# Kernel tuning notes

Hardware: AMD Instinct MI355X
Metric: run time of the kernel (lower is better)

The kernel has to match this reference:

```python
import jax, jax.numpy as jnp
import numpy as np

N_NODES = 10000
LN_EPS = 1e-5


def _gcn(x, W, b, src, dst):
    # GraphConvolution: linear transform then sum-aggregate messages over edges.
    sup = x @ W                               # [B, N, H]
    msg = sup[:, src, :]                      # [B, E, H] gather from source nodes
    agg = jax.vmap(lambda m: jax.ops.segment_sum(m, dst, num_segments=N_NODES))(msg)
    return agg + b


def _layernorm(x, g, b):
    mu = jnp.mean(x, axis=-1, keepdims=True)
    var = jnp.var(x, axis=-1, keepdims=True)
    return (x - mu) * jax.lax.rsqrt(var + LN_EPS) * g + b


def _attention_pool(x, W, u, num_iterations=3):
    # x: [B, N, d] -> r: [B, 1, d]
    a = jnp.tanh(x @ W) @ u                   # [B, N]
    alpha = jax.nn.softmax(a, axis=1)
    r = jnp.einsum('bn,bnd->bd', alpha, x)
    for _ in range(num_iterations):
        beta = jax.nn.softmax(jnp.einsum('bnd,bd->bn', x, r), axis=1)
        r = jnp.einsum('bn,bnd->bd', beta, x)
    return r[:, None, :]


def _forward(x, src, dst, W_conv0, b_conv0, W_convs, b_convs,
             mW1, mb1, mW2, mb2, mW3, mb3,
             ln1_g, ln1_b, ln2_g, ln2_b, attnW, attnu, fW1, fb1, fW2, fb2,
             fcW, fcb):
    gelu = lambda t: jax.nn.gelu(t, approximate=False)
    # stacked GCN layers (first layer distinct input dim)
    x = gelu(_gcn(x, W_conv0, b_conv0, src, dst))
    for i in range(W_convs.shape[0]):
        x = gelu(_gcn(x, W_convs[i], b_convs[i], src, dst))
    # dropout is identity in eval mode
    # MLP head
    x = jax.nn.relu(x @ mW1 + mb1)
    x = jax.nn.relu(x @ mW2 + mb2)
    x = x @ mW3 + mb3
    # Encoder: 2 layers of (attention-pool residual + LN + FFN residual + LN)
    for i in range(2):
        x = x + _attention_pool(x, attnW[i], attnu[i])   # broadcast [B,1,d]
        x = _layernorm(x, ln1_g[i], ln1_b[i])
        h = jax.nn.relu(x @ fW1[i] + fb1[i]) @ fW2[i] + fb2[i]
        x = _layernorm(x + h, ln2_g[i], ln2_b[i])
    x = x @ fcW + fcb                          # [B, N, out]
    return x.mean(axis=1)                      # [B, out]


def setup_inputs() -> dict:
    key = jax.random.key(0)
    ks = jax.random.split(key, 32)
    B, N, E = 4, N_NODES, 160000
    F_in, H, D, A, OUT = 128, 256, 256, 8, 10
    s = lambda k, *shape: jax.random.normal(k, shape, jnp.float32) * 0.05
    return {
        'x': jax.random.normal(ks[0], (B, N, F_in), jnp.float32),
        'src': jax.random.randint(ks[1], (E,), 0, N, jnp.int32),
        'dst': jax.random.randint(ks[2], (E,), 0, N, jnp.int32),
        'W_conv0': s(ks[3], F_in, H), 'b_conv0': s(ks[4], H),
        'W_convs': s(ks[5], 3, H, H), 'b_convs': s(ks[6], 3, H),
        'mW1': s(ks[7], H, H // 2), 'mb1': s(ks[8], H // 2),
        'mW2': s(ks[9], H // 2, H // 4), 'mb2': s(ks[10], H // 4),
        'mW3': s(ks[11], H // 4, D), 'mb3': s(ks[12], D),
        'ln1_g': jnp.ones((2, D), jnp.float32), 'ln1_b': jnp.zeros((2, D), jnp.float32),
        'ln2_g': jnp.ones((2, D), jnp.float32), 'ln2_b': jnp.zeros((2, D), jnp.float32),
        'attnW': s(ks[13], 2, D, A), 'attnu': s(ks[14], 2, A),
        'fW1': s(ks[15], 2, D, H), 'fb1': s(ks[16], 2, H),
        'fW2': s(ks[17], 2, H, D), 'fb2': s(ks[18], 2, D),
        'fcW': s(ks[19], D, OUT), 'fcb': s(ks[20], OUT),
    }


def reference(x, src, dst, W_conv0, b_conv0, W_convs, b_convs,
              mW1, mb1, mW2, mb2, mW3, mb3,
              ln1_g, ln1_b, ln2_g, ln2_b, attnW, attnu, fW1, fb1, fW2, fb2,
              fcW, fcb):
    return _forward(x, src, dst, W_conv0, b_conv0, W_convs, b_convs,
                    mW1, mb1, mW2, mb2, mW3, mb3,
                    ln1_g, ln1_b, ln2_g, ln2_b, attnW, attnu, fW1, fb1, fW2, fb2,
                    fcW, fcb)
```

## Files before the change

### kernel.cpp

```cpp
#include <hip/hip_runtime.h>
#include <math.h>

#define NN 10000
#define NB 4
#define NE 160000
#define DM 256
#define MR (NB * NN)
#define LN_EPS 1e-5f
#define WCHUNK 100
#define NCH (NN / WCHUNK)

typedef __attribute__((ext_vector_type(8))) short short8;
typedef __attribute__((ext_vector_type(8))) unsigned short us8;
typedef __attribute__((ext_vector_type(4))) float floatx4;


__device__ inline float bf2f(unsigned short u) {
    unsigned int x = ((unsigned int)u) << 16;
    float f;
    __builtin_memcpy(&f, &x, 4);
    return f;
}

__device__ inline unsigned short f2bf(float f) {
    unsigned int x;
    __builtin_memcpy(&x, &f, 4);
    unsigned int r = x + 0x7FFFu + ((x >> 16) & 1u);
    return (unsigned short)(r >> 16);
}

__device__ inline float gelu_exact(float x) {
    return 0.5f * x * (1.0f + erff(x * 0.70710678118654752f));
}

__device__ inline float waveAllReduce(float v) {
#pragma unroll
    for (int off = 32; off > 0; off >>= 1) v += __shfl_xor(v, off, 64);
    return v;
}

__device__ inline void gld16(const unsigned short* g, unsigned short* l) {
    __builtin_amdgcn_global_load_lds((const __attribute__((address_space(1))) void*)g,
                                     (__attribute__((address_space(3))) void*)l, 16, 0, 0);
}


__global__ void zero_f32_kernel(float* p, int n) {
    int i = blockIdx.x * 256 + threadIdx.x;
    if (i < n) p[i] = 0.0f;
}

__global__ void zero_i32_kernel(int* p, int n) {
    int i = blockIdx.x * 256 + threadIdx.x;
    if (i < n) p[i] = 0;
}

__global__ void cvt_bf16_kernel(const float* __restrict__ in, unsigned short* __restrict__ out, int n) {
    int i = blockIdx.x * 256 + threadIdx.x;
    if (i < n) out[i] = f2bf(in[i]);
}

struct TD { const float* src; unsigned short* dst; int K; int N; };
struct TDs { TD d[11]; };

__global__ void transpose_all_kernel(TDs tds) {
    TD t = tds.d[blockIdx.y];
    int idx = blockIdx.x * 256 + threadIdx.x;
    int total = t.K * t.N;
    if (idx < total) {
        int n = idx / t.K;
        int k = idx - n * t.K;
        t.dst[idx] = f2bf(t.src[(size_t)k * t.N + n]);
    }
}


__global__ void hist_kernel(const int* __restrict__ dst, int* __restrict__ counts, int e) {
    int i = blockIdx.x * 256 + threadIdx.x;
    if (i < e) atomicAdd(&counts[dst[i]], 1);
}

__global__ __launch_bounds__(256) void scan_kernel(const int* __restrict__ counts,
                                                   int* __restrict__ row_ptr,
                                                   int* __restrict__ fill_pos, int n) {
    __shared__ int sums[256];
    int tid = threadIdx.x;
    int chunk = (n + 255) / 256;
    int s0 = tid * chunk;
    int s1 = min(n, s0 + chunk);
    int local = 0;
    for (int i = s0; i < s1; i++) local += counts[i];
    sums[tid] = local;
    __syncthreads();
    for (int off = 1; off < 256; off <<= 1) {
        int v = (tid >= off) ? sums[tid - off] : 0;
        __syncthreads();
        sums[tid] += v;
        __syncthreads();
    }
    int base = (tid == 0) ? 0 : sums[tid - 1];
    for (int i = s0; i < s1; i++) {
        row_ptr[i] = base;
        fill_pos[i] = base;
        base += counts[i];
    }
    if (tid == 255) row_ptr[n] = sums[255];
}

__global__ void fill_kernel(const int* __restrict__ src, const int* __restrict__ dst,
                            int* __restrict__ fill_pos, int* __restrict__ csr_src, int e) {
    int i = blockIdx.x * 256 + threadIdx.x;
    if (i < e) {
        int p = atomicAdd(&fill_pos[dst[i]], 1);
        csr_src[p] = src[i];
    }
}


template <int BN, int CM>
__global__ __launch_bounds__(256) void mfma_gemm_kernel(
    const unsigned short* __restrict__ A, const unsigned short* __restrict__ Bt,
    const float* __restrict__ bias, void* __restrict__ Cp, int K, int N, int act) {
    constexpr int NBF = BN / 32;
    __shared__ unsigned short AsL[4 * 64 * 8];
    __shared__ unsigned short BsL[(BN / 16) * 64 * 8];

    const int tid = threadIdx.x;
    const int w = tid >> 6, l = tid & 63;
    const int wm = w >> 1, wn = w & 1;
    const int bm0 = blockIdx.y * 64;
    const int bn0 = blockIdx.x * BN;
    const int lm = l & 15, lq = l >> 4;

    floatx4 acc[2][NBF];
#pragma unroll
    for (int mi = 0; mi < 2; mi++)
#pragma unroll
        for (int ni = 0; ni < NBF; ni++) acc[mi][ni] = (floatx4){0.f, 0.f, 0.f, 0.f};

    const int s_ll = tid & 63;
    const int a_row = bm0 + (tid >> 6) * 16 + (s_ll & 15);
    const int s_kc = (s_ll >> 4) * 8;

    for (int k0 = 0; k0 < K; k0 += 32) {
        gld16(&A[(size_t)a_row * K + k0 + s_kc], &AsL[tid * 8]);
#pragma unroll
        for (int cc = 0; cc < BN / 64; cc++) {
            int c = tid + cc * 256;
            int rown = bn0 + (c >> 6) * 16 + (c & 15);
            int kc = k0 + ((c & 63) >> 4) * 8;
            gld16(&Bt[(size_t)rown * K + kc], &BsL[c * 8]);
        }
        __syncthreads();
        short8 af[2], bfv[NBF];
#pragma unroll
        for (int mi = 0; mi < 2; mi++) af[mi] = *(short8*)&AsL[((wm * 2 + mi) * 64 + l) * 8];
#pragma unroll
        for (int ni = 0; ni < NBF; ni++) bfv[ni] = *(short8*)&BsL[((wn * NBF + ni) * 64 + l) * 8];
#pragma unroll
        for (int mi = 0; mi < 2; mi++)
#pragma unroll
            for (int ni = 0; ni < NBF; ni++)
                acc[mi][ni] = __builtin_amdgcn_mfma_f32_16x16x32_bf16(af[mi], bfv[ni], acc[mi][ni], 0, 0, 0);
        __syncthreads();
    }

#pragma unroll
    for (int ni = 0; ni < NBF; ni++) {
        int col = bn0 + (wn * NBF + ni) * 16 + lm;
        float bv = bias ? bias[col] : 0.0f;
#pragma unroll
        for (int mi = 0; mi < 2; mi++) {
            int row0 = bm0 + (wm * 2 + mi) * 16 + lq * 4;
#pragma unroll
            for (int r = 0; r < 4; r++) {
                int row = row0 + r;
                float v = acc[mi][ni][r] + bv;
                if (act) v = fmaxf(v, 0.0f);
                if (CM == 0) {
                    ((float*)Cp)[(size_t)row * N + col] = v;
                } else if (CM == 1) {
                    ((unsigned short*)Cp)[(size_t)row * N + col] = f2bf(v);
                } else {
                    int bb = row / NN;
                    int nn = row - bb * NN;
                    ((unsigned short*)Cp)[(size_t)nn * (NB * DM) + bb * DM + col] = f2bf(v);
                }
            }
        }
    }
}


__global__ __launch_bounds__(256) void agg_kernel(const unsigned short* __restrict__ sup,
                                                  const int* __restrict__ row_ptr,
                                                  const int* __restrict__ csr_src,
                                                  const float* __restrict__ bias,
                                                  unsigned short* __restrict__ out) {
    int half = threadIdx.x >> 7;
    int n = blockIdx.x * 2 + half;
    int t = threadIdx.x & 127;
    int s = row_ptr[n], e = row_ptr[n + 1];
    float acc[8] = {0.f, 0.f, 0.f, 0.f, 0.f, 0.f, 0.f, 0.f};
    int j = s;
    for (; j + 4 <= e; j += 4) {
        int s0 = csr_src[j], s1 = csr_src[j + 1], s2 = csr_src[j + 2], s3 = csr_src[j + 3];
        us8 v0 = *(const us8*)&sup[(size_t)s0 * (NB * DM) + t * 8];
        us8 v1 = *(const us8*)&sup[(size_t)s1 * (NB * DM) + t * 8];
        us8 v2 = *(const us8*)&sup[(size_t)s2 * (NB * DM) + t * 8];
        us8 v3 = *(const us8*)&sup[(size_t)s3 * (NB * DM) + t * 8];
#pragma unroll
        for (int k = 0; k < 8; k++)
            acc[k] += (bf2f(v0[k]) + bf2f(v1[k])) + (bf2f(v2[k]) + bf2f(v3[k]));
    }
    for (; j < e; j++) {
        us8 v = *(const us8*)&sup[(size_t)csr_src[j] * (NB * DM) + t * 8];
#pragma unroll
        for (int k = 0; k < 8; k++) acc[k] += bf2f(v[k]);
    }
    int b = t >> 5, d0 = (t & 31) * 8;
    us8 o;
#pragma unroll
    for (int k = 0; k < 8; k++) o[k] = f2bf(gelu_exact(acc[k] + bias[d0 + k]));
    *(us8*)&out[((size_t)b * NN + n) * DM + d0] = o;
}


__global__ __launch_bounds__(256) void attn_score_kernel(const unsigned short* __restrict__ x16,
                                                         const float* __restrict__ W,
                                                         const float* __restrict__ u,
                                                         float* __restrict__ s) {
    int l = threadIdx.x & 63, w = threadIdx.x >> 6;
    int idx = blockIdx.x * 4 + w;
    ushort4 xb = *(const ushort4*)&x16[(size_t)idx * DM + l * 4];
    float xs[4] = {bf2f(xb.x), bf2f(xb.y), bf2f(xb.z), bf2f(xb.w)};
    const float4* Wv = (const float4*)W;
    int d0 = l * 4;
    float t[8] = {0, 0, 0, 0, 0, 0, 0, 0};
#pragma unroll
    for (int dd = 0; dd < 4; dd++) {
        float4 w0 = Wv[(d0 + dd) * 2 + 0];
        float4 w1 = Wv[(d0 + dd) * 2 + 1];
        t[0] += xs[dd] * w0.x; t[1] += xs[dd] * w0.y; t[2] += xs[dd] * w0.z; t[3] += xs[dd] * w0.w;
        t[4] += xs[dd] * w1.x; t[5] += xs[dd] * w1.y; t[6] += xs[dd] * w1.z; t[7] += xs[dd] * w1.w;
    }
#pragma unroll
    for (int j = 0; j < 8; j++) t[j] = waveAllReduce(t[j]);
    if (l == 0) {
        float acc = 0.0f;
#pragma unroll
        for (int j = 0; j < 8; j++) acc += tanhf(t[j]) * u[j];
        s[idx] = acc;
    }
}

__global__ __launch_bounds__(256) void dot_kernel(const unsigned short* __restrict__ x16,
                                                  const float* __restrict__ r,
                                                  float* __restrict__ s) {
    int l = threadIdx.x & 63, w = threadIdx.x >> 6;
    int idx = blockIdx.x * 4 + w;
    int b = idx / NN;
    ushort4 xb = *(const ushort4*)&x16[(size_t)idx * DM + l * 4];
    float4 rv = *(const float4*)&r[b * DM + l * 4];
    float acc = bf2f(xb.x) * rv.x + bf2f(xb.y) * rv.y + bf2f(xb.z) * rv.z + bf2f(xb.w) * rv.w;
    acc = waveAllReduce(acc);
    if (l == 0) s[idx] = acc;
}

__global__ __launch_bounds__(256) void attn_pool_kernel(const unsigned short* __restrict__ x16,
                                                        const float* __restrict__ sarr,
                                                        float* __restrict__ pm,
                                                        float* __restrict__ pl,
                                                        float* __restrict__ pv) {
    int c = blockIdx.x, b = blockIdx.y;
    int tid = threadIdx.x, w = tid >> 6, l = tid & 63;
    int n0 = c * WCHUNK;
    float m = -INFINITY, L = 0.0f;
    float v0 = 0.f, v1 = 0.f, v2 = 0.f, v3 = 0.f;
    for (int n = n0 + w; n < n0 + WCHUNK; n += 4) {
        float s = sarr[b * NN + n];
        ushort4 xb = *(const ushort4*)&x16[((size_t)b * NN + n) * DM + l * 4];
        float x0 = bf2f(xb.x), x1 = bf2f(xb.y), x2 = bf2f(xb.z), x3 = bf2f(xb.w);
        if (s > m) {
            float sc = __expf(m - s);
            L *= sc; v0 *= sc; v1 *= sc; v2 *= sc; v3 *= sc;
            m = s;
        }
        float wgt = __expf(s - m);
        L += wgt;
        v0 += wgt * x0; v1 += wgt * x1; v2 += wgt * x2; v3 += wgt * x3;
    }
    __shared__ float sm[4], sl[4];
    __shared__ float sv[4][DM];
    if (l == 0) { sm[w] = m; sl[w] = L; }
    float4 vv = {v0, v1, v2, v3};
    *(float4*)&sv[w][l * 4] = vv;
    __syncthreads();
    int d = tid;
    float M = fmaxf(fmaxf(sm[0], sm[1]), fmaxf(sm[2], sm[3]));
    float e0 = __expf(sm[0] - M), e1 = __expf(sm[1] - M);
    float e2 = __expf(sm[2] - M), e3 = __expf(sm[3] - M);
    float Lt = e0 * sl[0] + e1 * sl[1] + e2 * sl[2] + e3 * sl[3];
    float vd = e0 * sv[0][d] + e1 * sv[1][d] + e2 * sv[2][d] + e3 * sv[3][d];
    pv[((size_t)b * NCH + c) * DM + d] = vd;
    if (d == 0) {
        pm[b * NCH + c] = M;
        pl[b * NCH + c] = Lt;
    }
}

__global__ __launch_bounds__(256) void attn_combine_kernel(const float* __restrict__ pm,
                                                           const float* __restrict__ pl,
                                                           const float* __restrict__ pv,
                                                           float* __restrict__ r) {
    int b = blockIdx.x, tid = threadIdx.x;
    __shared__ float red[256];
    __shared__ float se[NCH];
    float mv = (tid < NCH) ? pm[b * NCH + tid] : -INFINITY;
    red[tid] = mv;
    __syncthreads();
    for (int off = 128; off > 0; off >>= 1) {
        if (tid < off) red[tid] = fmaxf(red[tid], red[tid + off]);
        __syncthreads();
    }
    float M = red[0];
    __syncthreads();
    float e = (tid < NCH) ? __expf(mv - M) : 0.0f;
    if (tid < NCH) se[tid] = e;
    red[tid] = (tid < NCH) ? e * pl[b * NCH + tid] : 0.0f;
    __syncthreads();
    for (int off = 128; off > 0; off >>= 1) {
        if (tid < off) red[tid] += red[tid + off];
        __syncthreads();
    }
    float L = red[0];
    __syncthreads();
    float acc = 0.0f;
    for (int c = 0; c < NCH; c++) acc += se[c] * pv[((size_t)b * NCH + c) * DM + tid];
    r[b * DM + tid] = acc / L;
}


__global__ __launch_bounds__(256) void ln_bcast_kernel(const unsigned short* __restrict__ x16,
                                                       const float* __restrict__ r,
                                                       const float* __restrict__ g,
                                                       const float* __restrict__ bt,
                                                       unsigned short* __restrict__ out16) {
    int l = threadIdx.x & 63, w = threadIdx.x >> 6;
    int row = blockIdx.x * 4 + w;
    int b = row / NN;
    ushort4 xb = *(const ushort4*)&x16[(size_t)row * DM + l * 4];
    float4 rv = *(const float4*)(r + (size_t)b * DM + l * 4);
    float4 y;
    y.x = bf2f(xb.x) + rv.x; y.y = bf2f(xb.y) + rv.y;
    y.z = bf2f(xb.z) + rv.z; y.w = bf2f(xb.w) + rv.w;
    float s = y.x + y.y + y.z + y.w;
    float sq = y.x * y.x + y.y * y.y + y.z * y.z + y.w * y.w;
    s = waveAllReduce(s);
    sq = waveAllReduce(sq);
    float mean = s * (1.0f / 256.0f);
    float var = sq * (1.0f / 256.0f) - mean * mean;
    float rstd = rsqrtf(var + LN_EPS);
    float4 gv = *(const float4*)(g + l * 4);
    float4 bv = *(const float4*)(bt + l * 4);
    ushort4 o;
    o.x = f2bf((y.x - mean) * rstd * gv.x + bv.x);
    o.y = f2bf((y.y - mean) * rstd * gv.y + bv.y);
    o.z = f2bf((y.z - mean) * rstd * gv.z + bv.z);
    o.w = f2bf((y.w - mean) * rstd * gv.w + bv.w);
    *(ushort4*)&out16[(size_t)row * DM + l * 4] = o;
}

__global__ __launch_bounds__(256) void ln_elem_kernel(const unsigned short* __restrict__ x16,
                                                      const float* __restrict__ h,
                                                      const float* __restrict__ g,
                                                      const float* __restrict__ bt,
                                                      unsigned short* __restrict__ out16) {
    int l = threadIdx.x & 63, w = threadIdx.x >> 6;
    int row = blockIdx.x * 4 + w;
    ushort4 xb = *(const ushort4*)&x16[(size_t)row * DM + l * 4];
    float4 hv = *(const float4*)(h + (size_t)row * DM + l * 4);
    float4 y;
    y.x = bf2f(xb.x) + hv.x; y.y = bf2f(xb.y) + hv.y;
    y.z = bf2f(xb.z) + hv.z; y.w = bf2f(xb.w) + hv.w;
    float s = y.x + y.y + y.z + y.w;
    float sq = y.x * y.x + y.y * y.y + y.z * y.z + y.w * y.w;
    s = waveAllReduce(s);
    sq = waveAllReduce(sq);
    float mean = s * (1.0f / 256.0f);
    float var = sq * (1.0f / 256.0f) - mean * mean;
    float rstd = rsqrtf(var + LN_EPS);
    float4 gv = *(const float4*)(g + l * 4);
    float4 bv = *(const float4*)(bt + l * 4);
    ushort4 o;
    o.x = f2bf((y.x - mean) * rstd * gv.x + bv.x);
    o.y = f2bf((y.y - mean) * rstd * gv.y + bv.y);
    o.z = f2bf((y.z - mean) * rstd * gv.z + bv.z);
    o.w = f2bf((y.w - mean) * rstd * gv.w + bv.w);
    *(ushort4*)&out16[(size_t)row * DM + l * 4] = o;
}


__global__ __launch_bounds__(256) void colsum_kernel(const unsigned short* __restrict__ x16,
                                                     float* __restrict__ cs) {
    int b = blockIdx.y, c = blockIdx.x, d = threadIdx.x;
    int n0 = c * WCHUNK, n1 = n0 + WCHUNK;
    float acc = 0.0f;
    for (int n = n0; n < n1; n++) acc += bf2f(x16[((size_t)b * NN + n) * DM + d]);
    atomicAdd(&cs[b * DM + d], acc);
}

__global__ __launch_bounds__(64) void final_kernel(const float* __restrict__ cs,
                                                   const float* __restrict__ fcW,
                                                   const float* __restrict__ fcb,
                                                   float* __restrict__ out) {
    int b = blockIdx.x;
    int o = threadIdx.x;
    if (o < 10) {
        float acc = 0.0f;
        for (int d = 0; d < DM; d++) acc += cs[b * DM + d] * fcW[d * 10 + o];
        out[b * 10 + o] = acc * (1.0f / NN) + fcb[o];
    }
}


extern "C" void kernel_launch(void* const* d_in, const int* in_sizes, int n_in,
                              void* d_out, int out_size, void* d_ws, size_t ws_size,
                              hipStream_t stream) {
    const float* x_in    = (const float*)d_in[0];
    const int*   src     = (const int*)d_in[1];
    const int*   dst     = (const int*)d_in[2];
    const float* W_conv0 = (const float*)d_in[3];
    const float* b_conv0 = (const float*)d_in[4];
    const float* W_convs = (const float*)d_in[5];
    const float* b_convs = (const float*)d_in[6];
    const float* mW1 = (const float*)d_in[7];
    const float* mb1 = (const float*)d_in[8];
    const float* mW2 = (const float*)d_in[9];
    const float* mb2 = (const float*)d_in[10];
    const float* mW3 = (const float*)d_in[11];
    const float* mb3 = (const float*)d_in[12];
    const float* ln1_g = (const float*)d_in[13];
    const float* ln1_b = (const float*)d_in[14];
    const float* ln2_g = (const float*)d_in[15];
    const float* ln2_b = (const float*)d_in[16];
    const float* attnW = (const float*)d_in[17];
    const float* attnu = (const float*)d_in[18];
    const float* fW1 = (const float*)d_in[19];
    const float* fb1 = (const float*)d_in[20];
    const float* fW2 = (const float*)d_in[21];
    const float* fb2 = (const float*)d_in[22];
    const float* fcW = (const float*)d_in[23];
    const float* fcb = (const float*)d_in[24];
    float* out = (float*)d_out;

    char* p = (char*)d_ws;
    auto alloc = [&](size_t bytes) { char* q = p; p += (bytes + 255) & ~(size_t)255; return q; };
    float* A = (float*)alloc((size_t)MR * DM * 4);
    unsigned short* sup16 = (unsigned short*)alloc((size_t)MR * DM * 2);
    unsigned short* act16 = (unsigned short*)alloc((size_t)MR * DM * 2);
    unsigned short* b16   = (unsigned short*)alloc((size_t)MR * DM * 2);
    unsigned short* t1    = (unsigned short*)alloc((size_t)MR * 128 * 2);
    unsigned short* t2    = (unsigned short*)alloc((size_t)MR * 64 * 2);
    unsigned short* wt    = (unsigned short*)alloc((size_t)548864 * 2);
    float* a_score = (float*)alloc((size_t)MR * 4);
    float* rbuf = (float*)alloc(NB * DM * 4);
    float* pm0  = (float*)alloc(NB * NCH * 4);
    float* pl0  = (float*)alloc(NB * NCH * 4);
    float* pv0  = (float*)alloc((size_t)NB * NCH * DM * 4);
    float* colsum = (float*)alloc(NB * DM * 4);
    int* counts   = (int*)alloc(NN * 4);
    int* row_ptr  = (int*)alloc((NN + 1) * 4);
    int* fill_pos = (int*)alloc(NN * 4);
    int* csr_src  = (int*)alloc(NE * 4);

    unsigned short* Wt_conv0 = wt;
    unsigned short* Wt_convs = Wt_conv0 + 32768;
    unsigned short* mW1t = Wt_convs + 196608;
    unsigned short* mW2t = mW1t + 32768;
    unsigned short* mW3t = mW2t + 8192;
    unsigned short* fW1t = mW3t + 16384;
    unsigned short* fW2t = fW1t + 131072;

    const dim3 blk(256);

    zero_i32_kernel<<<(NN + 255) / 256, blk, 0, stream>>>(counts, NN);
    hist_kernel<<<(NE + 255) / 256, blk, 0, stream>>>(dst, counts, NE);
    scan_kernel<<<1, blk, 0, stream>>>(counts, row_ptr, fill_pos, NN);
    fill_kernel<<<(NE + 255) / 256, blk, 0, stream>>>(src, dst, fill_pos, csr_src, NE);

    TDs tds;
    tds.d[0]  = {W_conv0, Wt_conv0, 128, 256};
    tds.d[1]  = {W_convs + 0 * 65536, Wt_convs + 0 * 65536, 256, 256};
    tds.d[2]  = {W_convs + 1 * 65536, Wt_convs + 1 * 65536, 256, 256};
    tds.d[3]  = {W_convs + 2 * 65536, Wt_convs + 2 * 65536, 256, 256};
    tds.d[4]  = {mW1, mW1t, 256, 128};
    tds.d[5]  = {mW2, mW2t, 128, 64};
    tds.d[6]  = {mW3, mW3t, 64, 256};
    tds.d[7]  = {fW1 + 0 * 65536, fW1t + 0 * 65536, 256, 256};
    tds.d[8]  = {fW1 + 1 * 65536, fW1t + 1 * 65536, 256, 256};
    tds.d[9]  = {fW2 + 0 * 65536, fW2t + 0 * 65536, 256, 256};
    tds.d[10] = {fW2 + 1 * 65536, fW2t + 1 * 65536, 256, 256};
    transpose_all_kernel<<<dim3(256, 11), blk, 0, stream>>>(tds);

    cvt_bf16_kernel<<<(MR * 128 + 255) / 256, blk, 0, stream>>>(x_in, t1, MR * 128);

    mfma_gemm_kernel<128, 2><<<dim3(2, MR / 64), blk, 0, stream>>>(t1, Wt_conv0, nullptr, sup16, 128, 256, 0);
    agg_kernel<<<NN / 2, blk, 0, stream>>>(sup16, row_ptr, csr_src, b_conv0, act16);
    for (int i = 0; i < 3; i++) {
        mfma_gemm_kernel<128, 2><<<dim3(2, MR / 64), blk, 0, stream>>>(act16, Wt_convs + (size_t)i * 65536, nullptr, sup16, 256, 256, 0);
        agg_kernel<<<NN / 2, blk, 0, stream>>>(sup16, row_ptr, csr_src, b_convs + (size_t)i * 256, act16);
    }

    mfma_gemm_kernel<128, 1><<<dim3(1, MR / 64), blk, 0, stream>>>(act16, mW1t, mb1, t1, 256, 128, 1);
    mfma_gemm_kernel<64, 1><<<dim3(1, MR / 64), blk, 0, stream>>>(t1, mW2t, mb2, t2, 128, 64, 1);
    mfma_gemm_kernel<128, 1><<<dim3(2, MR / 64), blk, 0, stream>>>(t2, mW3t, mb3, act16, 64, 256, 0);

    const dim3 poolGrid(NCH, NB);
    for (int i = 0; i < 2; i++) {
        const float* Wp = attnW + (size_t)i * DM * 8;
        const float* up = attnu + (size_t)i * 8;
        attn_score_kernel<<<MR / 4, blk, 0, stream>>>(act16, Wp, up, a_score);
        attn_pool_kernel<<<poolGrid, blk, 0, stream>>>(act16, a_score, pm0, pl0, pv0);
        attn_combine_kernel<<<NB, blk, 0, stream>>>(pm0, pl0, pv0, rbuf);
        for (int it = 0; it < 3; it++) {
            dot_kernel<<<MR / 4, blk, 0, stream>>>(act16, rbuf, a_score);
            attn_pool_kernel<<<poolGrid, blk, 0, stream>>>(act16, a_score, pm0, pl0, pv0);
            attn_combine_kernel<<<NB, blk, 0, stream>>>(pm0, pl0, pv0, rbuf);
        }
        ln_bcast_kernel<<<MR / 4, blk, 0, stream>>>(act16, rbuf, ln1_g + (size_t)i * DM,
                                                    ln1_b + (size_t)i * DM, b16);
        mfma_gemm_kernel<128, 1><<<dim3(2, MR / 64), blk, 0, stream>>>(b16, fW1t + (size_t)i * 65536,
                                                                       fb1 + (size_t)i * DM, sup16, 256, 256, 1);
        mfma_gemm_kernel<128, 0><<<dim3(2, MR / 64), blk, 0, stream>>>(sup16, fW2t + (size_t)i * 65536,
                                                                       fb2 + (size_t)i * DM, A, 256, 256, 0);
        ln_elem_kernel<<<MR / 4, blk, 0, stream>>>(b16, A, ln2_g + (size_t)i * DM,
                                                   ln2_b + (size_t)i * DM, act16);
    }

    zero_f32_kernel<<<4, blk, 0, stream>>>(colsum, NB * DM);
    colsum_kernel<<<poolGrid, blk, 0, stream>>>(act16, colsum);
    final_kernel<<<NB, dim3(64), 0, stream>>>(colsum, fcW, fcb, out);
}
```

Baseline: 879.3 us.

## Raise parallelism in GCN aggregation and attention-pool chunking

The aggregation kernel now gives each node a whole 256-thread block, with one wave per batch item reading 4 bf16 per lane, and unrolls the edge loop by 8 so more gathers are in flight. The attention pool uses smaller chunks (25 nodes instead of 100), which launches 4x more blocks. The combine kernel now loops over the 400 partials per thread to handle the larger count. Both changes aim to raise occupancy and latency hiding on memory-bound gather and reduction work, in exchange for more blocks, narrower loads and more partials to combine.

New measurement: 895.3 us. No clear change (+1.8%).

```diff
diff --git a/kernel.cpp b/kernel.cpp
--- a/kernel.cpp
+++ b/kernel.cpp
@@ -7,8 +7,9 @@
 #define DM 256
 #define MR (NB * NN)
 #define LN_EPS 1e-5f
-#define WCHUNK 100
-#define NCH (NN / WCHUNK)
+#define PCH 25
+#define NCH (NN / PCH)
+#define CCH 100
 
 typedef __attribute__((ext_vector_type(8))) short short8;
 typedef __attribute__((ext_vector_type(8))) unsigned short us8;
@@ -197,32 +198,37 @@
                                                   const int* __restrict__ csr_src,
                                                   const float* __restrict__ bias,
                                                   unsigned short* __restrict__ out) {
-    int half = threadIdx.x >> 7;
-    int n = blockIdx.x * 2 + half;
-    int t = threadIdx.x & 127;
+    int n = blockIdx.x;
+    int w = threadIdx.x >> 6, l = threadIdx.x & 63;
     int s = row_ptr[n], e = row_ptr[n + 1];
-    float acc[8] = {0.f, 0.f, 0.f, 0.f, 0.f, 0.f, 0.f, 0.f};
+    const int off = w * DM + l * 4;
+    float a0 = 0.f, a1 = 0.f, a2 = 0.f, a3 = 0.f;
     int j = s;
-    for (; j + 4 <= e; j += 4) {
-        int s0 = csr_src[j], s1 = csr_src[j + 1], s2 = csr_src[j + 2], s3 = csr_src[j + 3];
-        us8 v0 = *(const us8*)&sup[(size_t)s0 * (NB * DM) + t * 8];
-        us8 v1 = *(const us8*)&sup[(size_t)s1 * (NB * DM) + t * 8];
-        us8 v2 = *(const us8*)&sup[(size_t)s2 * (NB * DM) + t * 8];
-        us8 v3 = *(const us8*)&sup[(size_t)s3 * (NB * DM) + t * 8];
-#pragma unroll
-        for (int k = 0; k < 8; k++)
-            acc[k] += (bf2f(v0[k]) + bf2f(v1[k])) + (bf2f(v2[k]) + bf2f(v3[k]));
+    for (; j + 8 <= e; j += 8) {
+        int idx[8];
+#pragma unroll
+        for (int k = 0; k < 8; k++) idx[k] = csr_src[j + k];
+        ushort4 v[8];
+#pragma unroll
+        for (int k = 0; k < 8; k++) v[k] = *(const ushort4*)&sup[(size_t)idx[k] * (NB * DM) + off];
+#pragma unroll
+        for (int k = 0; k < 8; k++) {
+            a0 += bf2f(v[k].x); a1 += bf2f(v[k].y);
+            a2 += bf2f(v[k].z); a3 += bf2f(v[k].w);
+        }
     }
     for (; j < e; j++) {
-        us8 v = *(const us8*)&sup[(size_t)csr_src[j] * (NB * DM) + t * 8];
-#pragma unroll
-        for (int k = 0; k < 8; k++) acc[k] += bf2f(v[k]);
-    }
-    int b = t >> 5, d0 = (t & 31) * 8;
-    us8 o;
-#pragma unroll
-    for (int k = 0; k < 8; k++) o[k] = f2bf(gelu_exact(acc[k] + bias[d0 + k]));
-    *(us8*)&out[((size_t)b * NN + n) * DM + d0] = o;
+        ushort4 v = *(const ushort4*)&sup[(size_t)csr_src[j] * (NB * DM) + off];
+        a0 += bf2f(v.x); a1 += bf2f(v.y); a2 += bf2f(v.z); a3 += bf2f(v.w);
+    }
+    int d0 = l * 4;
+    const float4 bv = *(const float4*)&bias[d0];
+    ushort4 o;
+    o.x = f2bf(gelu_exact(a0 + bv.x));
+    o.y = f2bf(gelu_exact(a1 + bv.y));
+    o.z = f2bf(gelu_exact(a2 + bv.z));
+    o.w = f2bf(gelu_exact(a3 + bv.w));
+    *(ushort4*)&out[((size_t)w * NN + n) * DM + d0] = o;
 }
 
 
@@ -274,10 +280,10 @@
                                                         float* __restrict__ pv) {
     int c = blockIdx.x, b = blockIdx.y;
     int tid = threadIdx.x, w = tid >> 6, l = tid & 63;
-    int n0 = c * WCHUNK;
+    int n0 = c * PCH;
     float m = -INFINITY, L = 0.0f;
     float v0 = 0.f, v1 = 0.f, v2 = 0.f, v3 = 0.f;
-    for (int n = n0 + w; n < n0 + WCHUNK; n += 4) {
+    for (int n = n0 + w; n < n0 + PCH; n += 4) {
         float s = sarr[b * NN + n];
         ushort4 xb = *(const ushort4*)&x16[((size_t)b * NN + n) * DM + l * 4];
         float x0 = bf2f(xb.x), x1 = bf2f(xb.y), x2 = bf2f(xb.z), x3 = bf2f(xb.w);
@@ -316,7 +322,8 @@
     int b = blockIdx.x, tid = threadIdx.x;
     __shared__ float red[256];
     __shared__ float se[NCH];
-    float mv = (tid < NCH) ? pm[b * NCH + tid] : -INFINITY;
+    float mv = -INFINITY;
+    for (int c = tid; c < NCH; c += 256) mv = fmaxf(mv, pm[b * NCH + c]);
     red[tid] = mv;
     __syncthreads();
     for (int off = 128; off > 0; off >>= 1) {
@@ -325,9 +332,13 @@
     }
     float M = red[0];
     __syncthreads();
-    float e = (tid < NCH) ? __expf(mv - M) : 0.0f;
-    if (tid < NCH) se[tid] = e;
-    red[tid] = (tid < NCH) ? e * pl[b * NCH + tid] : 0.0f;
+    float lsum = 0.0f;
+    for (int c = tid; c < NCH; c += 256) {
+        float e = __expf(pm[b * NCH + c] - M);
+        se[c] = e;
+        lsum += e * pl[b * NCH + c];
+    }
+    red[tid] = lsum;
     __syncthreads();
     for (int off = 128; off > 0; off >>= 1) {
         if (tid < off) red[tid] += red[tid + off];
@@ -404,7 +415,7 @@
 __global__ __launch_bounds__(256) void colsum_kernel(const unsigned short* __restrict__ x16,
                                                      float* __restrict__ cs) {
     int b = blockIdx.y, c = blockIdx.x, d = threadIdx.x;
-    int n0 = c * WCHUNK, n1 = n0 + WCHUNK;
+    int n0 = c * CCH, n1 = n0 + CCH;
     float acc = 0.0f;
     for (int n = n0; n < n1; n++) acc += bf2f(x16[((size_t)b * NN + n) * DM + d]);
     atomicAdd(&cs[b * DM + d], acc);
@@ -506,10 +517,10 @@
     cvt_bf16_kernel<<<(MR * 128 + 255) / 256, blk, 0, stream>>>(x_in, t1, MR * 128);
 
     mfma_gemm_kernel<128, 2><<<dim3(2, MR / 64), blk, 0, stream>>>(t1, Wt_conv0, nullptr, sup16, 128, 256, 0);
-    agg_kernel<<<NN / 2, blk, 0, stream>>>(sup16, row_ptr, csr_src, b_conv0, act16);
+    agg_kernel<<<NN, blk, 0, stream>>>(sup16, row_ptr, csr_src, b_conv0, act16);
     for (int i = 0; i < 3; i++) {
         mfma_gemm_kernel<128, 2><<<dim3(2, MR / 64), blk, 0, stream>>>(act16, Wt_convs + (size_t)i * 65536, nullptr, sup16, 256, 256, 0);
-        agg_kernel<<<NN / 2, blk, 0, stream>>>(sup16, row_ptr, csr_src, b_convs + (size_t)i * 256, act16);
+        agg_kernel<<<NN, blk, 0, stream>>>(sup16, row_ptr, csr_src, b_convs + (size_t)i * 256, act16);
     }
 
     mfma_gemm_kernel<128, 1><<<dim3(1, MR / 64), blk, 0, stream>>>(act16, mW1t, mb1, t1, 256, 128, 1);
@@ -539,6 +550,6 @@
     }
 
     zero_f32_kernel<<<4, blk, 0, stream>>>(colsum, NB * DM);
-    colsum_kernel<<<poolGrid, blk, 0, stream>>>(act16, colsum);
+    colsum_kernel<<<dim3(NN / CCH, NB), blk, 0, stream>>>(act16, colsum);
     final_kernel<<<NB, dim3(64), 0, stream>>>(colsum, fcW, fcb, out);
 }
```
